# Performance work log

Hardware: AMD Instinct MI355X
Metric: run time of the kernel (lower is better)

## Reference

```python
import jax, jax.numpy as jnp
import numpy as np

EPS = 1e-6  # torch.nn.PairwiseDistance default eps: dist = ||x - y + eps||_2


def setup_inputs() -> dict:
    key = jax.random.key(0)
    k1, k2 = jax.random.split(key)
    samples = jax.random.normal(k1, (4096, 128), dtype=jnp.float32)   # batch of observations
    V = jax.random.uniform(k2, (65536, 128), dtype=jnp.float32)       # grown node codebook (torch.rand init)
    return {"samples": samples, "V": V}


def reference(samples, V):
    # activate_bmu, vectorized over the batch.
    # torch PairwiseDistance(p=2): d_n = || x - V_n + eps ||_2
    D = samples.shape[-1]
    x_sq = jnp.sum(samples * samples, axis=-1)        # [B]
    v_sq = jnp.sum(V * V, axis=-1)                    # [N]
    xv = jnp.einsum('bd,nd->bn', samples, V)          # [B, N]
    x_sum = jnp.sum(samples, axis=-1)                 # [B]
    v_sum = jnp.sum(V, axis=-1)                       # [N]
    sq = (x_sq[:, None] + v_sq[None, :] - 2.0 * xv
          + 2.0 * EPS * (x_sum[:, None] - v_sum[None, :]) + D * EPS * EPS)
    dists = jnp.sqrt(jnp.maximum(sq, 0.0))            # [B, N]
    # top-2 smallest distances -> BMU b, second BMU s
    neg_top2, idx = jax.lax.top_k(-dists, 2)          # [B, 2]
    b = idx[:, 0]
    s = idx[:, 1]
    a = jnp.exp(neg_top2[:, 0])                       # exp(-b_dist)
    return (b, s, a)
```

## Files before the change

### kernel.cpp

```cpp
#include <hip/hip_runtime.h>
#include <math.h>

#define NS 4096
#define NV 65536
#define DDIM 128
#define EPSV 1e-6f
#define NCHUNK 16
#define TILES_PER_CHUNK 32
#define NTILE 512
#define FLTMAX 3.402823466e+38f
#define IMAX 0x7fffffff

#define XSQ_F    0
#define XSUM_F   4096
#define PART_F   8192
#define D12_F    270336
#define T12_I    278528
#define CELL1_I  286720
#define CELL2_I  290816
#define WS_TILED_BYTE 1605632
#define TILE_BYTES 65536
#define TILE_STRIDE 66560

typedef __attribute__((ext_vector_type(8)))  __bf16        bf16x8;
typedef __attribute__((ext_vector_type(8)))  unsigned short ush8;
typedef __attribute__((ext_vector_type(4)))  unsigned short ush4;
typedef __attribute__((ext_vector_type(16))) float          f32x16;

typedef const __attribute__((address_space(1))) unsigned int* gp_t;
typedef __attribute__((address_space(3))) unsigned int*       lp_t;

__device__ __forceinline__ void async_cp16(const void* g, void* l) {
    __builtin_amdgcn_global_load_lds((gp_t)g, (lp_t)l, 16, 0, 0);
}

__device__ __forceinline__ unsigned short f2bf(float x) {
    unsigned u = __builtin_bit_cast(unsigned, x);
    u += 0x7FFFu + ((u >> 16) & 1u);
    return (unsigned short)(u >> 16);
}
__device__ __forceinline__ float bf2f(unsigned short h) {
    unsigned u = ((unsigned)h) << 16;
    return __builtin_bit_cast(float, u);
}

__device__ __forceinline__ void merge2t(float& d1, int& i1, float& d2, int& i2,
                                        float d, int i) {
    bool b1 = (d < d1) || (d == d1 && i < i1);
    bool b2 = (d < d2) || (d == d2 && i < i2);
    if (b1) { d2 = d1; i2 = i1; d1 = d; i1 = i; }
    else if (b2) { d2 = d; i2 = i; }
}

__device__ __forceinline__ void load_bfrag(const float* __restrict__ samples,
                                           int srow, int q, ush8* bh, ush8* bl) {
    const float4* s4 = (const float4*)samples;
    #pragma unroll
    for (int s = 0; s < 8; s++) {
        float4 x0 = s4[(size_t)srow * 32 + s * 4 + q * 2];
        float4 x1 = s4[(size_t)srow * 32 + s * 4 + q * 2 + 1];
        float xs[8] = {x0.x, x0.y, x0.z, x0.w, x1.x, x1.y, x1.z, x1.w};
        #pragma unroll
        for (int j = 0; j < 8; j++) {
            float y = -2.0f * xs[j];
            unsigned short hh = f2bf(y);
            bh[s][j] = hh;
            bl[s][j] = f2bf(y - bf2f(hh));
        }
    }
}

__device__ __forceinline__ void cvt_sample_piece(const float4* __restrict__ s4,
                                                 int srcrow, int row, int kq,
                                                 char* lds) {
    float4 xv = s4[(size_t)srcrow * 32 + kq];
    int k0 = kq * 4, sI = k0 >> 4, qI = (k0 >> 3) & 1, j0 = k0 & 7;
    float xs[4] = {xv.x, xv.y, xv.z, xv.w};
    ush4 h, l;
    #pragma unroll
    for (int e = 0; e < 4; e++) {
        float y = -2.0f * xs[e];
        unsigned short hh = f2bf(y);
        h[e] = hh;
        l[e] = f2bf(y - bf2f(hh));
    }
    *(ush4*)(lds + ((((sI * 2 + 0) * 2 + qI) * 128) + row) * 16 + j0 * 2) = h;
    *(ush4*)(lds + ((((sI * 2 + 1) * 2 + qI) * 128) + row) * 16 + j0 * 2) = l;
}

__device__ __forceinline__ void tile_mfma(const char* __restrict__ base,
                                          const ush8* bh, const ush8* bl,
                                          int q, int l31, f32x16 acc[4]) {
    #pragma unroll
    for (int mi = 0; mi < 4; mi++) {
        const char* cjb = base + TILE_BYTES + (size_t)(mi * 32 + 4 * q) * 4;
        float4 c0 = *(const float4*)(cjb);
        float4 c1 = *(const float4*)(cjb + 32);
        float4 c2 = *(const float4*)(cjb + 64);
        float4 c3 = *(const float4*)(cjb + 96);
        acc[mi][0] = c0.x;  acc[mi][1] = c0.y;  acc[mi][2] = c0.z;  acc[mi][3] = c0.w;
        acc[mi][4] = c1.x;  acc[mi][5] = c1.y;  acc[mi][6] = c1.z;  acc[mi][7] = c1.w;
        acc[mi][8] = c2.x;  acc[mi][9] = c2.y;  acc[mi][10] = c2.z; acc[mi][11] = c2.w;
        acc[mi][12] = c3.x; acc[mi][13] = c3.y; acc[mi][14] = c3.z; acc[mi][15] = c3.w;
    }
    #pragma unroll
    for (int s = 0; s < 8; s++) {
        bf16x8 bhs = __builtin_bit_cast(bf16x8, bh[s]);
        bf16x8 bls = __builtin_bit_cast(bf16x8, bl[s]);
        #pragma unroll
        for (int mi = 0; mi < 4; mi++) {
            bf16x8 ah = *(const bf16x8*)(base + (size_t)((((s * 2 + 0) * 2 + q) * 128) + mi * 32 + l31) * 16);
            bf16x8 al = *(const bf16x8*)(base + (size_t)((((s * 2 + 1) * 2 + q) * 128) + mi * 32 + l31) * 16);
            acc[mi] = __builtin_amdgcn_mfma_f32_32x32x16_bf16(ah, bhs, acc[mi], 0, 0, 0);
            acc[mi] = __builtin_amdgcn_mfma_f32_32x32x16_bf16(ah, bls, acc[mi], 0, 0, 0);
            acc[mi] = __builtin_amdgcn_mfma_f32_32x32x16_bf16(al, bhs, acc[mi], 0, 0, 0);
        }
    }
}

__global__ void vq_prep(const float* __restrict__ samples,
                        const float* __restrict__ V,
                        char* __restrict__ ws) {
    __shared__ float tf[128 * 132];
    float* ws_f = (float*)ws;
    const int b = blockIdx.x;
    const int tid = threadIdx.x;
    if (b >= NV / 128) {
        int row = (b - NV / 128) * 4 + (tid >> 6);
        int lane = tid & 63;
        float2 v = ((const float2*)(samples + (size_t)row * DDIM))[lane];
        float s = v.x + v.y;
        float q = v.x * v.x + v.y * v.y;
        #pragma unroll
        for (int off = 32; off >= 1; off >>= 1) {
            s += __shfl_xor(s, off);
            q += __shfl_xor(q, off);
        }
        if (lane == 0) { ws_f[XSQ_F + row] = q; ws_f[XSUM_F + row] = s; }
        return;
    }
    const int tile = b;
    char* dst = ws + WS_TILED_BYTE + (size_t)tile * TILE_STRIDE;
    const float4* v4 = (const float4*)V;
    #pragma unroll
    for (int i = 0; i < 16; i++) {
        int flat = i * 256 + tid;
        int row = flat >> 5;
        int c4 = flat & 31;
        float4 g = v4[(size_t)(tile * 128 + row) * 32 + c4];
        *(float4*)&tf[row * 132 + c4 * 4] = g;
        float s = g.x + g.y + g.z + g.w;
        float q2 = g.x * g.x + g.y * g.y + g.z * g.z + g.w * g.w;
        #pragma unroll
        for (int off = 16; off >= 1; off >>= 1) {
            s += __shfl_xor(s, off);
            q2 += __shfl_xor(q2, off);
        }
        if ((tid & 31) == 0)
            *(float*)(dst + TILE_BYTES + row * 4) = q2 - 2.0f * EPSV * s;
    }
    __syncthreads();
    #pragma unroll
    for (int i = 0; i < 8; i++) {
        int task = i * 256 + tid;
        int row = task & 127;
        int sq = task >> 7;
        int s = sq >> 1, q = sq & 1;
        float4 lo = *(const float4*)&tf[row * 132 + s * 16 + q * 8];
        float4 hi = *(const float4*)&tf[row * 132 + s * 16 + q * 8 + 4];
        float xs[8] = {lo.x, lo.y, lo.z, lo.w, hi.x, hi.y, hi.z, hi.w};
        ush8 h, l;
        #pragma unroll
        for (int j = 0; j < 8; j++) {
            unsigned short hh = f2bf(xs[j]);
            h[j] = hh;
            l[j] = f2bf(xs[j] - bf2f(hh));
        }
        *(ush8*)(dst + (size_t)((((s * 2 + 0) * 2 + q) * 128) + row) * 16) = h;
        *(ush8*)(dst + (size_t)((((s * 2 + 1) * 2 + q) * 128) + row) * 16) = l;
    }
}

__global__ __launch_bounds__(512, 2)
void vq_gemm_topk(const float* __restrict__ samples, char* __restrict__ ws) {
    __shared__ __align__(16) char lds[TILE_BYTES];
    const int tid = threadIdx.x;
    const int w = tid >> 6, lane = tid & 63;
    const int l31 = lane & 31, qb = lane >> 5;
    const int mi_own = w & 3;
    const int sh = w >> 2;
    const int bid = blockIdx.x;
    const int g = bid >> 3;
    const int chunk = (bid & 7) * 2 + (g >> 5);
    const int st = g & 31;

    const float4* s4 = (const float4*)samples;
    #pragma unroll
    for (int i = 0; i < 8; i++) {
        int flat = i * 512 + tid;
        int row = flat >> 5, kq = flat & 31;
        cvt_sample_piece(s4, st * 128 + row, row, kq, lds);
    }
    __syncthreads();

    const char* vbase = ws + WS_TILED_BYTE;
    const int tbase = chunk * TILES_PER_CHUNK;

    float D1a = FLTMAX, D2a = FLTMAX, D1b = FLTMAX, D2b = FLTMAX;
    int T1a = IMAX, T2a = IMAX, T1b = IMAX, T2b = IMAX;

    #pragma unroll 1
    for (int it = 0; it < TILES_PER_CHUNK; it++) {
        const int tile = tbase + it;
        const char* tsrc = vbase + (size_t)tile * TILE_STRIDE;
        const char* cjb = tsrc + TILE_BYTES + (size_t)(mi_own * 32 + 4 * qb) * 4;
        float4 c0 = *(const float4*)(cjb);
        float4 c1 = *(const float4*)(cjb + 32);
        float4 c2 = *(const float4*)(cjb + 64);
        float4 c3 = *(const float4*)(cjb + 96);
        f32x16 acc0, acc1;
        acc0[0] = c0.x;  acc0[1] = c0.y;  acc0[2] = c0.z;  acc0[3] = c0.w;
        acc0[4] = c1.x;  acc0[5] = c1.y;  acc0[6] = c1.z;  acc0[7] = c1.w;
        acc0[8] = c2.x;  acc0[9] = c2.y;  acc0[10] = c2.z; acc0[11] = c2.w;
        acc0[12] = c3.x; acc0[13] = c3.y; acc0[14] = c3.z; acc0[15] = c3.w;
        acc1 = acc0;
        #pragma unroll
        for (int hs = 0; hs < 2; hs++) {
            ush8 ah[4], al[4];
            #pragma unroll
            for (int si = 0; si < 4; si++) {
                int s = hs * 4 + si;
                ah[si] = *(const ush8*)(tsrc + (size_t)((((s * 2 + 0) * 2 + qb) * 128) + mi_own * 32 + l31) * 16);
                al[si] = *(const ush8*)(tsrc + (size_t)((((s * 2 + 1) * 2 + qb) * 128) + mi_own * 32 + l31) * 16);
            }
            #pragma unroll
            for (int si = 0; si < 4; si++) {
                int s = hs * 4 + si;
                bf16x8 a_h = __builtin_bit_cast(bf16x8, ah[si]);
                bf16x8 a_l = __builtin_bit_cast(bf16x8, al[si]);
                bf16x8 b0h = *(const bf16x8*)(lds + (size_t)((((s * 2 + 0) * 2 + qb) * 128) + sh * 64 + l31) * 16);
                bf16x8 b0l = *(const bf16x8*)(lds + (size_t)((((s * 2 + 1) * 2 + qb) * 128) + sh * 64 + l31) * 16);
                bf16x8 b1h = *(const bf16x8*)(lds + (size_t)((((s * 2 + 0) * 2 + qb) * 128) + sh * 64 + 32 + l31) * 16);
                bf16x8 b1l = *(const bf16x8*)(lds + (size_t)((((s * 2 + 1) * 2 + qb) * 128) + sh * 64 + 32 + l31) * 16);
                acc0 = __builtin_amdgcn_mfma_f32_32x32x16_bf16(a_h, b0h, acc0, 0, 0, 0);
                acc0 = __builtin_amdgcn_mfma_f32_32x32x16_bf16(a_h, b0l, acc0, 0, 0, 0);
                acc0 = __builtin_amdgcn_mfma_f32_32x32x16_bf16(a_l, b0h, acc0, 0, 0, 0);
                acc1 = __builtin_amdgcn_mfma_f32_32x32x16_bf16(a_h, b1h, acc1, 0, 0, 0);
                acc1 = __builtin_amdgcn_mfma_f32_32x32x16_bf16(a_h, b1l, acc1, 0, 0, 0);
                acc1 = __builtin_amdgcn_mfma_f32_32x32x16_bf16(a_l, b1h, acc1, 0, 0, 0);
            }
        }
        {
            float t1 = FLTMAX, t2 = FLTMAX;
            #pragma unroll
            for (int r = 0; r < 16; r++) {
                float v = acc0[r];
                t2 = __builtin_amdgcn_fmed3f(t1, t2, v);
                t1 = fminf(t1, v);
            }
            bool c1 = t1 < D1a;
            float m1 = fminf(D1a, t2);
            float m2 = fminf(D2a, t1);
            int T2x = (t2 < D1a) ? tile : T1a;
            int T2y = (t1 < D2a) ? tile : T2a;
            D2a = c1 ? m1 : m2;
            T2a = c1 ? T2x : T2y;
            T1a = c1 ? tile : T1a;
            D1a = c1 ? t1 : D1a;
        }
        {
            float t1 = FLTMAX, t2 = FLTMAX;
            #pragma unroll
            for (int r = 0; r < 16; r++) {
                float v = acc1[r];
                t2 = __builtin_amdgcn_fmed3f(t1, t2, v);
                t1 = fminf(t1, v);
            }
            bool c1 = t1 < D1b;
            float m1 = fminf(D1b, t2);
            float m2 = fminf(D2b, t1);
            int T2x = (t2 < D1b) ? tile : T1b;
            int T2y = (t1 < D2b) ? tile : T2b;
            D2b = c1 ? m1 : m2;
            T2b = c1 ? T2x : T2y;
            T1b = c1 ? tile : T1b;
            D1b = c1 ? t1 : D1b;
        }
    }

    {
        float od1 = __shfl_xor(D1a, 32), od2 = __shfl_xor(D2a, 32);
        int   ot1 = __shfl_xor(T1a, 32), ot2 = __shfl_xor(T2a, 32);
        merge2t(D1a, T1a, D2a, T2a, od1, ot1);
        merge2t(D1a, T1a, D2a, T2a, od2, ot2);
    }
    {
        float od1 = __shfl_xor(D1b, 32), od2 = __shfl_xor(D2b, 32);
        int   ot1 = __shfl_xor(T1b, 32), ot2 = __shfl_xor(T2b, 32);
        merge2t(D1b, T1b, D2b, T2b, od1, ot1);
        merge2t(D1b, T1b, D2b, T2b, od2, ot2);
    }
    __syncthreads();
    float4* scratch = (float4*)lds;
    if (qb == 0) {
        scratch[mi_own * 128 + sh * 64 + l31]      = make_float4(D1a, D2a, (float)T1a, (float)T2a);
        scratch[mi_own * 128 + sh * 64 + 32 + l31] = make_float4(D1b, D2b, (float)T1b, (float)T2b);
    }
    __syncthreads();
    if (mi_own == 0 && qb == 0) {
        float4* part = (float4*)((float*)ws + PART_F);
        #pragma unroll
        for (int gg = 0; gg < 2; gg++) {
            int sidx = sh * 64 + gg * 32 + l31;
            float4 p0 = scratch[sidx];
            float d1 = p0.x, d2 = p0.y;
            int t1 = (int)p0.z, t2 = (int)p0.w;
            #pragma unroll
            for (int mm = 1; mm < 4; mm++) {
                float4 p = scratch[mm * 128 + sidx];
                merge2t(d1, t1, d2, t2, p.x, (int)p.z);
                merge2t(d1, t1, d2, t2, p.y, (int)p.w);
            }
            part[(size_t)(st * 128 + sidx) * NCHUNK + chunk] =
                make_float4(d1, d2, (float)t1, (float)t2);
        }
    }
}

__global__ void vq_merge(float* __restrict__ ws_f, float* __restrict__ out) {
    const int m = blockIdx.x * 256 + threadIdx.x;
    int* ws_i = (int*)ws_f;
    const float4* part = (const float4*)(ws_f + PART_F);
    float d1 = FLTMAX, d2 = FLTMAX;
    int t1 = IMAX, t2 = IMAX;
    #pragma unroll
    for (int c = 0; c < NCHUNK; c++) {
        float4 p = part[(size_t)m * NCHUNK + c];
        merge2t(d1, t1, d2, t2, p.x, (int)p.z);
        merge2t(d1, t1, d2, t2, p.y, (int)p.w);
    }
    ((float2*)(ws_f + D12_F))[m] = make_float2(d1, d2);
    ((int2*)(ws_i + T12_I))[m] = make_int2(t1, t2);
    ws_i[CELL1_I + m] = IMAX;
    ws_i[CELL2_I + m] = IMAX;
    float ci = ws_f[XSQ_F + m] + 2.0f * EPSV * ws_f[XSUM_F + m] + (float)DDIM * EPSV * EPSV;
    out[2 * NS + m] = expf(-sqrtf(fmaxf(ci + d1, 0.0f)));
}

__global__ __launch_bounds__(256)
void vq_recover(const float* __restrict__ samples, char* __restrict__ ws) {
    __shared__ __align__(16) char sbuf[TILE_STRIDE];
    __shared__ int list[NS];
    __shared__ int lcnt;
    const int tid = threadIdx.x;
    const int w = tid >> 6, lane = tid & 63;
    const int l31 = lane & 31, qb = lane >> 5;
    const int tile = blockIdx.x;
    int* ws_i = (int*)ws;
    float* ws_f = (float*)ws;

    const char* tsrc = ws + WS_TILED_BYTE + (size_t)tile * TILE_STRIDE;
    #pragma unroll
    for (int i = 0; i < 16; i++) {
        int off = (i * 256 + tid) * 16;
        async_cp16(tsrc + off, sbuf + off);
    }
    if (tid < 64) {
        int off = TILE_BYTES + tid * 16;
        async_cp16(tsrc + off, sbuf + off);
    }
    if (tid == 0) lcnt = 0;
    __syncthreads();
    const int2* t12 = (const int2*)(ws_i + T12_I);
    for (int i = tid; i < NS; i += 256) {
        int2 t = t12[i];
        if (t.x == tile || t.y == tile) {
            int p = atomicAdd(&lcnt, 1);
            list[p] = i;
        }
    }
    __syncthreads();
    const int cnt = lcnt;
    if (cnt == 0) return;

    const float2* d12 = (const float2*)(ws_f + D12_F);
    const float nanf_ = __int_as_float(0x7fc00000);

    for (int b0 = 0; b0 < cnt; b0 += 128) {
        int li = b0 + w * 32 + l31;
        bool valid = li < cnt;
        int m = valid ? list[li] : 0;
        ush8 bh[8], bl[8];
        load_bfrag(samples, m, qb, bh, bl);
        float d1t = nanf_, d2t = nanf_;
        if (valid) {
            float2 dt = d12[m];
            d1t = dt.x; d2t = dt.y;
        }
        f32x16 acc[4];
        tile_mfma(sbuf, bh, bl, qb, l31, acc);
        #pragma unroll
        for (int mi = 0; mi < 4; mi++) {
            #pragma unroll
            for (int r = 0; r < 16; r++) {
                float v = acc[mi][r];
                int idx = tile * 128 + mi * 32 + (r & 3) + 8 * (r >> 2) + 4 * qb;
                if (v == d1t) {
                    int old = atomicMin(&ws_i[CELL1_I + m], idx);
                    int loser = old > idx ? old : idx;
                    atomicMin(&ws_i[CELL2_I + m], loser);
                } else if (v == d2t) {
                    atomicMin(&ws_i[CELL2_I + m], idx);
                }
            }
        }
    }
}

__global__ void vq_finalize(const char* __restrict__ ws, float* __restrict__ out) {
    const int m = blockIdx.x * 256 + threadIdx.x;
    const int* ws_i = (const int*)ws;
    out[m]      = (float)ws_i[CELL1_I + m];
    out[NS + m] = (float)ws_i[CELL2_I + m];
}

extern "C" void kernel_launch(void* const* d_in, const int* in_sizes, int n_in,
                              void* d_out, int out_size, void* d_ws, size_t ws_size,
                              hipStream_t stream) {
    (void)in_sizes; (void)n_in; (void)out_size; (void)ws_size;
    const float* samples = (const float*)d_in[0];
    const float* V = (const float*)d_in[1];
    float* out = (float*)d_out;
    float* ws_f = (float*)d_ws;
    char*  ws_b = (char*)d_ws;

    vq_prep<<<dim3(NV / 128 + NS / 4), 256, 0, stream>>>(samples, V, ws_b);
    vq_gemm_topk<<<dim3((NS / 128) * NCHUNK), 512, 0, stream>>>(samples, ws_b);
    vq_merge<<<dim3(NS / 256), 256, 0, stream>>>(ws_f, out);
    vq_recover<<<dim3(NTILE), 256, 0, stream>>>(samples, ws_b);
    vq_finalize<<<dim3(NS / 256), 256, 0, stream>>>(ws_b, out);
}
```

Baseline: 349.6 us.

## Double-buffer codebook tiles in LDS with async copies, keep samples in registers

The GEMM-topk kernel now uses 1024-thread blocks, each covering 256 samples. Each wave holds its sample B-fragments (hi/lo bf16 split) in registers. Codebook tiles are streamed into two LDS buffers with async copies, so the next tile loads while MFMAs run on the current one, instead of each wave reading A fragments straight from global memory. The per-block reduction is simpler, but grid size halves, occupancy falls to one block per CU, and register pressure from the held fragments rises.

```diff
diff --git a/kernel.cpp b/kernel.cpp
--- a/kernel.cpp
+++ b/kernel.cpp
@@ -68,24 +68,6 @@
             bl[s][j] = f2bf(y - bf2f(hh));
         }
     }
-}
-
-__device__ __forceinline__ void cvt_sample_piece(const float4* __restrict__ s4,
-                                                 int srcrow, int row, int kq,
-                                                 char* lds) {
-    float4 xv = s4[(size_t)srcrow * 32 + kq];
-    int k0 = kq * 4, sI = k0 >> 4, qI = (k0 >> 3) & 1, j0 = k0 & 7;
-    float xs[4] = {xv.x, xv.y, xv.z, xv.w};
-    ush4 h, l;
-    #pragma unroll
-    for (int e = 0; e < 4; e++) {
-        float y = -2.0f * xs[e];
-        unsigned short hh = f2bf(y);
-        h[e] = hh;
-        l[e] = f2bf(y - bf2f(hh));
-    }
-    *(ush4*)(lds + ((((sI * 2 + 0) * 2 + qI) * 128) + row) * 16 + j0 * 2) = h;
-    *(ush4*)(lds + ((((sI * 2 + 1) * 2 + qI) * 128) + row) * 16 + j0 * 2) = l;
 }
 
 __device__ __forceinline__ void tile_mfma(const char* __restrict__ base,
@@ -181,75 +163,91 @@
     }
 }
 
-__global__ __launch_bounds__(512, 2)
+__device__ __forceinline__ void stage_tile1024(const char* src, char* l, int tid) {
+    #pragma unroll
+    for (int i = 0; i < 4; i++) {
+        int off = (i * 1024 + tid) * 16;
+        async_cp16(src + off, l + off);
+    }
+    if (tid < 64) {
+        int off = TILE_BYTES + tid * 16;
+        async_cp16(src + off, l + off);
+    }
+}
+
+__global__ __launch_bounds__(1024, 1)
 void vq_gemm_topk(const float* __restrict__ samples, char* __restrict__ ws) {
-    __shared__ __align__(16) char lds[TILE_BYTES];
+    __shared__ __align__(16) char lds[2][TILE_STRIDE];
+    __shared__ float4 pmerge[256];
     const int tid = threadIdx.x;
     const int w = tid >> 6, lane = tid & 63;
     const int l31 = lane & 31, qb = lane >> 5;
-    const int mi_own = w & 3;
-    const int sh = w >> 2;
+    const int si = w & 7;
+    const int ch = w >> 3;
     const int bid = blockIdx.x;
     const int g = bid >> 3;
-    const int chunk = (bid & 7) * 2 + (g >> 5);
-    const int st = g & 31;
-
-    const float4* s4 = (const float4*)samples;
-    #pragma unroll
-    for (int i = 0; i < 8; i++) {
-        int flat = i * 512 + tid;
-        int row = flat >> 5, kq = flat & 31;
-        cvt_sample_piece(s4, st * 128 + row, row, kq, lds);
-    }
-    __syncthreads();
+    const int chunk = (bid & 7) * 2 + (g >> 4);
+    const int st = g & 15;
+    const int nrow = st * 256 + si * 32 + l31;
 
     const char* vbase = ws + WS_TILED_BYTE;
     const int tbase = chunk * TILES_PER_CHUNK;
 
+    stage_tile1024(vbase + (size_t)tbase * TILE_STRIDE, lds[0], tid);
+    ush8 bh[8], bl[8];
+    load_bfrag(samples, nrow, qb, bh, bl);
+    __syncthreads();
+
     float D1a = FLTMAX, D2a = FLTMAX, D1b = FLTMAX, D2b = FLTMAX;
     int T1a = IMAX, T2a = IMAX, T1b = IMAX, T2b = IMAX;
+    const int mi0 = ch * 2, mi1 = ch * 2 + 1;
 
     #pragma unroll 1
     for (int it = 0; it < TILES_PER_CHUNK; it++) {
+        const int cur = it & 1;
+        if (it + 1 < TILES_PER_CHUNK)
+            stage_tile1024(vbase + (size_t)(tbase + it + 1) * TILE_STRIDE,
+                           lds[cur ^ 1], tid);
+        const char* base = lds[cur];
+        f32x16 acc0, acc1;
+        {
+            const char* cjb = base + TILE_BYTES + (size_t)(mi0 * 32 + 4 * qb) * 4;
+            float4 c0 = *(const float4*)(cjb);
+            float4 c1 = *(const float4*)(cjb + 32);
+            float4 c2 = *(const float4*)(cjb + 64);
+            float4 c3 = *(const float4*)(cjb + 96);
+            acc0[0] = c0.x;  acc0[1] = c0.y;  acc0[2] = c0.z;  acc0[3] = c0.w;
+            acc0[4] = c1.x;  acc0[5] = c1.y;  acc0[6] = c1.z;  acc0[7] = c1.w;
+            acc0[8] = c2.x;  acc0[9] = c2.y;  acc0[10] = c2.z; acc0[11] = c2.w;
+            acc0[12] = c3.x; acc0[13] = c3.y; acc0[14] = c3.z; acc0[15] = c3.w;
+        }
+        {
+            const char* cjb = base + TILE_BYTES + (size_t)(mi1 * 32 + 4 * qb) * 4;
+            float4 c0 = *(const float4*)(cjb);
+            float4 c1 = *(const float4*)(cjb + 32);
+            float4 c2 = *(const float4*)(cjb + 64);
+            float4 c3 = *(const float4*)(cjb + 96);
+            acc1[0] = c0.x;  acc1[1] = c0.y;  acc1[2] = c0.z;  acc1[3] = c0.w;
+            acc1[4] = c1.x;  acc1[5] = c1.y;  acc1[6] = c1.z;  acc1[7] = c1.w;
+            acc1[8] = c2.x;  acc1[9] = c2.y;  acc1[10] = c2.z; acc1[11] = c2.w;
+            acc1[12] = c3.x; acc1[13] = c3.y; acc1[14] = c3.z; acc1[15] = c3.w;
+        }
+        #pragma unroll
+        for (int s = 0; s < 8; s++) {
+            bf16x8 bhs = __builtin_bit_cast(bf16x8, bh[s]);
+            bf16x8 bls = __builtin_bit_cast(bf16x8, bl[s]);
+            bf16x8 ah0 = *(const bf16x8*)(base + (size_t)((((s * 2 + 0) * 2 + qb) * 128) + mi0 * 32 + l31) * 16);
+            bf16x8 al0 = *(const bf16x8*)(base + (size_t)((((s * 2 + 1) * 2 + qb) * 128) + mi0 * 32 + l31) * 16);
+            bf16x8 ah1 = *(const bf16x8*)(base + (size_t)((((s * 2 + 0) * 2 + qb) * 128) + mi1 * 32 + l31) * 16);
+            bf16x8 al1 = *(const bf16x8*)(base + (size_t)((((s * 2 + 1) * 2 + qb) * 128) + mi1 * 32 + l31) * 16);
+            acc0 = __builtin_amdgcn_mfma_f32_32x32x16_bf16(ah0, bhs, acc0, 0, 0, 0);
+            acc0 = __builtin_amdgcn_mfma_f32_32x32x16_bf16(ah0, bls, acc0, 0, 0, 0);
+            acc0 = __builtin_amdgcn_mfma_f32_32x32x16_bf16(al0, bhs, acc0, 0, 0, 0);
+            acc1 = __builtin_amdgcn_mfma_f32_32x32x16_bf16(ah1, bhs, acc1, 0, 0, 0);
+            acc1 = __builtin_amdgcn_mfma_f32_32x32x16_bf16(ah1, bls, acc1, 0, 0, 0);
+            acc1 = __builtin_amdgcn_mfma_f32_32x32x16_bf16(al1, bhs, acc1, 0, 0, 0);
+        }
         const int tile = tbase + it;
-        const char* tsrc = vbase + (size_t)tile * TILE_STRIDE;
-        const char* cjb = tsrc + TILE_BYTES + (size_t)(mi_own * 32 + 4 * qb) * 4;
-        float4 c0 = *(const float4*)(cjb);
-        float4 c1 = *(const float4*)(cjb + 32);
-        float4 c2 = *(const float4*)(cjb + 64);
-        float4 c3 = *(const float4*)(cjb + 96);
-        f32x16 acc0, acc1;
-        acc0[0] = c0.x;  acc0[1] = c0.y;  acc0[2] = c0.z;  acc0[3] = c0.w;
-        acc0[4] = c1.x;  acc0[5] = c1.y;  acc0[6] = c1.z;  acc0[7] = c1.w;
-        acc0[8] = c2.x;  acc0[9] = c2.y;  acc0[10] = c2.z; acc0[11] = c2.w;
-        acc0[12] = c3.x; acc0[13] = c3.y; acc0[14] = c3.z; acc0[15] = c3.w;
-        acc1 = acc0;
-        #pragma unroll
-        for (int hs = 0; hs < 2; hs++) {
-            ush8 ah[4], al[4];
-            #pragma unroll
-            for (int si = 0; si < 4; si++) {
-                int s = hs * 4 + si;
-                ah[si] = *(const ush8*)(tsrc + (size_t)((((s * 2 + 0) * 2 + qb) * 128) + mi_own * 32 + l31) * 16);
-                al[si] = *(const ush8*)(tsrc + (size_t)((((s * 2 + 1) * 2 + qb) * 128) + mi_own * 32 + l31) * 16);
-            }
-            #pragma unroll
-            for (int si = 0; si < 4; si++) {
-                int s = hs * 4 + si;
-                bf16x8 a_h = __builtin_bit_cast(bf16x8, ah[si]);
-                bf16x8 a_l = __builtin_bit_cast(bf16x8, al[si]);
-                bf16x8 b0h = *(const bf16x8*)(lds + (size_t)((((s * 2 + 0) * 2 + qb) * 128) + sh * 64 + l31) * 16);
-                bf16x8 b0l = *(const bf16x8*)(lds + (size_t)((((s * 2 + 1) * 2 + qb) * 128) + sh * 64 + l31) * 16);
-                bf16x8 b1h = *(const bf16x8*)(lds + (size_t)((((s * 2 + 0) * 2 + qb) * 128) + sh * 64 + 32 + l31) * 16);
-                bf16x8 b1l = *(const bf16x8*)(lds + (size_t)((((s * 2 + 1) * 2 + qb) * 128) + sh * 64 + 32 + l31) * 16);
-                acc0 = __builtin_amdgcn_mfma_f32_32x32x16_bf16(a_h, b0h, acc0, 0, 0, 0);
-                acc0 = __builtin_amdgcn_mfma_f32_32x32x16_bf16(a_h, b0l, acc0, 0, 0, 0);
-                acc0 = __builtin_amdgcn_mfma_f32_32x32x16_bf16(a_l, b0h, acc0, 0, 0, 0);
-                acc1 = __builtin_amdgcn_mfma_f32_32x32x16_bf16(a_h, b1h, acc1, 0, 0, 0);
-                acc1 = __builtin_amdgcn_mfma_f32_32x32x16_bf16(a_h, b1l, acc1, 0, 0, 0);
-                acc1 = __builtin_amdgcn_mfma_f32_32x32x16_bf16(a_l, b1h, acc1, 0, 0, 0);
-            }
-        }
         {
             float t1 = FLTMAX, t2 = FLTMAX;
             #pragma unroll
@@ -286,44 +284,27 @@
             T1b = c1 ? tile : T1b;
             D1b = c1 ? t1 : D1b;
         }
-    }
-
+        __syncthreads();
+    }
+
+    merge2t(D1a, T1a, D2a, T2a, D1b, T1b);
+    merge2t(D1a, T1a, D2a, T2a, D2b, T2b);
     {
         float od1 = __shfl_xor(D1a, 32), od2 = __shfl_xor(D2a, 32);
         int   ot1 = __shfl_xor(T1a, 32), ot2 = __shfl_xor(T2a, 32);
         merge2t(D1a, T1a, D2a, T2a, od1, ot1);
         merge2t(D1a, T1a, D2a, T2a, od2, ot2);
     }
-    {
-        float od1 = __shfl_xor(D1b, 32), od2 = __shfl_xor(D2b, 32);
-        int   ot1 = __shfl_xor(T1b, 32), ot2 = __shfl_xor(T2b, 32);
-        merge2t(D1b, T1b, D2b, T2b, od1, ot1);
-        merge2t(D1b, T1b, D2b, T2b, od2, ot2);
-    }
+    if (ch == 1 && qb == 0)
+        pmerge[si * 32 + l31] = make_float4(D1a, D2a, (float)T1a, (float)T2a);
     __syncthreads();
-    float4* scratch = (float4*)lds;
-    if (qb == 0) {
-        scratch[mi_own * 128 + sh * 64 + l31]      = make_float4(D1a, D2a, (float)T1a, (float)T2a);
-        scratch[mi_own * 128 + sh * 64 + 32 + l31] = make_float4(D1b, D2b, (float)T1b, (float)T2b);
-    }
-    __syncthreads();
-    if (mi_own == 0 && qb == 0) {
+    if (ch == 0 && qb == 0) {
+        float4 o = pmerge[si * 32 + l31];
+        merge2t(D1a, T1a, D2a, T2a, o.x, (int)o.z);
+        merge2t(D1a, T1a, D2a, T2a, o.y, (int)o.w);
         float4* part = (float4*)((float*)ws + PART_F);
-        #pragma unroll
-        for (int gg = 0; gg < 2; gg++) {
-            int sidx = sh * 64 + gg * 32 + l31;
-            float4 p0 = scratch[sidx];
-            float d1 = p0.x, d2 = p0.y;
-            int t1 = (int)p0.z, t2 = (int)p0.w;
-            #pragma unroll
-            for (int mm = 1; mm < 4; mm++) {
-                float4 p = scratch[mm * 128 + sidx];
-                merge2t(d1, t1, d2, t2, p.x, (int)p.z);
-                merge2t(d1, t1, d2, t2, p.y, (int)p.w);
-            }
-            part[(size_t)(st * 128 + sidx) * NCHUNK + chunk] =
-                make_float4(d1, d2, (float)t1, (float)t2);
-        }
+        part[(size_t)nrow * NCHUNK + chunk] =
+            make_float4(D1a, D2a, (float)T1a, (float)T2a);
     }
 }
 
@@ -435,7 +416,7 @@
     char*  ws_b = (char*)d_ws;
 
     vq_prep<<<dim3(NV / 128 + NS / 4), 256, 0, stream>>>(samples, V, ws_b);
-    vq_gemm_topk<<<dim3((NS / 128) * NCHUNK), 512, 0, stream>>>(samples, ws_b);
+    vq_gemm_topk<<<dim3((NS / 256) * NCHUNK), 1024, 0, stream>>>(samples, ws_b);
     vq_merge<<<dim3(NS / 256), 256, 0, stream>>>(ws_f, out);
     vq_recover<<<dim3(NTILE), 256, 0, stream>>>(samples, ws_b);
     vq_finalize<<<dim3(NS / 256), 256, 0, stream>>>(ws_b, out);
```

Result: no change. 344.6 us (-1.4%).
